# Optimization experiments

Hardware: AMD Instinct MI355X
Metric: run time of the kernel (lower is better)

## Reference

```python
import jax, jax.numpy as jnp
import numpy as np

N = 8192   # nodes
K = 64     # spectrum bins
DK = 64    # d_k == input_dim F'
G = 16     # num propagation modes
TAU = 1.0


def setup_inputs() -> dict:
    key = jax.random.key(0)
    ks = jax.random.split(key, 15)
    r = lambda k, sh, sc=1.0: jax.random.normal(k, sh, jnp.float32) * sc
    return {
        'z_n': r(ks[0], (N, DK)),
        'P_ref': r(ks[1], (N, K)),
        'P_in': r(ks[2], (N, K)),
        'A_ref': r(ks[3], (N, K)),
        'A_in': r(ks[4], (N, K)),
        'R_nm': r(ks[5], (N, N), 0.01),
        # learned params (torch nn.Linear stores weight as [out, in]; y = x @ W.T + b)
        'W_ind_w': r(ks[6], (DK, DK), 1.0 / np.sqrt(DK)),
        'W_ind_b': jnp.zeros((DK,), jnp.float32),
        'W_gate_w': r(ks[7], (DK, DK), 1.0 / np.sqrt(DK)),
        'W_gate_b': jnp.zeros((DK,), jnp.float32),
        'W_sys_w': r(ks[8], (DK, 2), 1.0 / np.sqrt(2.0)),
        'W_sys_b': jnp.zeros((DK,), jnp.float32),
        'W_s': r(ks[9], (G, DK, DK)),  # nn.Parameter(torch.randn(...))
        'W_k_w': r(ks[10], (DK, DK * DK), 1.0 / DK),
        'W_k_b': jnp.zeros((DK,), jnp.float32),
    }


def _delta(X_in, X_ref):
    # delta[i] = mean_{j,k} (X_in[j,k] - X_ref[i,k])^2 -> [N, 1]
    # (faithful to the broadcasted [N,N,K] mean in the torch code, computed
    #  via the expanded quadratic so the N^2*K tensor is never materialized)
    Kf = jnp.float32(X_in.shape[1])
    m_in2 = jnp.mean(X_in * X_in)              # scalar mean over j,k of X_in^2
    m_in = jnp.mean(X_in, axis=0)              # [K] mean over j
    d = m_in2 - 2.0 * (X_ref @ m_in) / Kf + jnp.mean(X_ref * X_ref, axis=1)
    return d[:, None]


def reference(z_n, P_ref, P_in, A_ref, A_in, R_nm,
              W_ind_w, W_ind_b, W_gate_w, W_gate_b,
              W_sys_w, W_sys_b, W_s, W_k_w, W_k_b):
    dP = _delta(P_in, P_ref)                                    # [N,1]
    dA = _delta(A_in, A_ref)                                    # [N,1]
    gate = jax.nn.sigmoid(z_n @ W_gate_w.T + W_gate_b)          # [N,DK]
    sys_feat = jnp.concatenate([dA, dP], axis=1) @ W_sys_w.T + W_sys_b
    q_n = z_n @ W_ind_w.T + W_ind_b + gate * sys_feat           # [N,DK]
    k_g = W_s.reshape(W_s.shape[0], -1) @ W_k_w.T + W_k_b       # [G,DK]
    s_ng = (q_n @ k_g.T) / jnp.sqrt(jnp.float32(DK))            # [N,G]
    u = jax.random.uniform(jax.random.key(42), s_ng.shape, jnp.float32)
    gumbel = -jnp.log(-jnp.log(u + 1e-10) + 1e-10)
    alpha = jax.nn.softmax((s_ng + gumbel) / TAU, axis=-1)      # [N,G]
    # fused: sum_g alpha[n,g] * (W_s[g] @ z_n[n])
    propagated = jnp.einsum('ng,gij,nj->ni', alpha, W_s, z_n)   # [N,DK]
    h_n = jax.nn.leaky_relu(R_nm @ propagated, negative_slope=0.01)
    return (h_n, s_ng)
```

## Files before the change

### kernel.cpp

```cpp
#include <hip/hip_runtime.h>
#include <hip/hip_bf16.h>
#include <stdint.h>

#define NN 8192

typedef __attribute__((ext_vector_type(8))) __bf16 bf16x8;
typedef __attribute__((ext_vector_type(4))) float f32x4;

#define WS_KG    192
#define WS_ALPHA 1216
#define WS_PT_BYTE 529408
#define WS_PART  394496
#define WS_KGP   427776

__device__ __forceinline__ void threefry2x32(uint32_t x0, uint32_t x1,
                                             uint32_t& o0, uint32_t& o1) {
  const uint32_t k0 = 0u, k1 = 42u;
  const uint32_t k2 = k0 ^ k1 ^ 0x1BD11BDAu;
  x0 += k0; x1 += k1;
#define TF_R(r) { x0 += x1; x1 = (x1 << (r)) | (x1 >> (32 - (r))); x1 ^= x0; }
  TF_R(13) TF_R(15) TF_R(26) TF_R(6)
  x0 += k1; x1 += k2 + 1u;
  TF_R(17) TF_R(29) TF_R(16) TF_R(24)
  x0 += k2; x1 += k0 + 2u;
  TF_R(13) TF_R(15) TF_R(26) TF_R(6)
  x0 += k0; x1 += k1 + 3u;
  TF_R(17) TF_R(29) TF_R(16) TF_R(24)
  x0 += k1; x1 += k2 + 4u;
  TF_R(13) TF_R(15) TF_R(26) TF_R(6)
  x0 += k2; x1 += k0 + 5u;
#undef TF_R
  o0 = x0; o1 = x1;
}

__device__ __forceinline__ bf16x8 cvt8(const float* __restrict__ p) {
  float4 a = *(const float4*)p;
  float4 b = *(const float4*)(p + 4);
  bf16x8 r;
  r[0] = (__bf16)a.x; r[1] = (__bf16)a.y; r[2] = (__bf16)a.z; r[3] = (__bf16)a.w;
  r[4] = (__bf16)b.x; r[5] = (__bf16)b.y; r[6] = (__bf16)b.z; r[7] = (__bf16)b.w;
  return r;
}

__device__ __forceinline__ bf16x8 cvt8g(const float* p) {
  float4 a = *(const float4*)p;
  float4 b = *(const float4*)(p + 4);
  bf16x8 r;
  r[0] = (__bf16)a.x; r[1] = (__bf16)a.y; r[2] = (__bf16)a.z; r[3] = (__bf16)a.w;
  r[4] = (__bf16)b.x; r[5] = (__bf16)b.y; r[6] = (__bf16)b.z; r[7] = (__bf16)b.w;
  return r;
}

__global__ __launch_bounds__(256) void k1_partial(const float* __restrict__ Pin,
                                                  const float* __restrict__ Ain,
                                                  float* __restrict__ ws) {
  __shared__ float scp[64], sca[64], ssq[2];
  int t = threadIdx.x, b = blockIdx.x;
  if (t < 64) { scp[t] = 0.f; sca[t] = 0.f; }
  if (t < 2) ssq[t] = 0.f;
  __syncthreads();
  const float4* P4 = (const float4*)Pin;
  const float4* A4 = (const float4*)Ain;
  float sp = 0.f, sa = 0.f;
  float cp0 = 0, cp1 = 0, cp2 = 0, cp3 = 0, ca0 = 0, ca1 = 0, ca2 = 0, ca3 = 0;
  int base = b * 512 + t;
#pragma unroll
  for (int k = 0; k < 2; ++k) {
    float4 p = P4[base + k * 256], a = A4[base + k * 256];
    sp += p.x * p.x + p.y * p.y + p.z * p.z + p.w * p.w;
    sa += a.x * a.x + a.y * a.y + a.z * a.z + a.w * a.w;
    cp0 += p.x; cp1 += p.y; cp2 += p.z; cp3 += p.w;
    ca0 += a.x; ca1 += a.y; ca2 += a.z; ca3 += a.w;
  }
  int c0 = (t * 4) & 63;
  atomicAdd(&scp[c0 + 0], cp0); atomicAdd(&scp[c0 + 1], cp1);
  atomicAdd(&scp[c0 + 2], cp2); atomicAdd(&scp[c0 + 3], cp3);
  atomicAdd(&sca[c0 + 0], ca0); atomicAdd(&sca[c0 + 1], ca1);
  atomicAdd(&sca[c0 + 2], ca2); atomicAdd(&sca[c0 + 3], ca3);
  for (int off = 32; off; off >>= 1) {
    sp += __shfl_down(sp, off);
    sa += __shfl_down(sa, off);
  }
  if ((t & 63) == 0) { atomicAdd(&ssq[0], sp); atomicAdd(&ssq[1], sa); }
  __syncthreads();
  float* dst = ws + WS_PART + b * 130;
  if (t < 64) { dst[2 + t] = scp[t]; dst[66 + t] = sca[t]; }
  if (t == 0) { dst[0] = ssq[0]; dst[1] = ssq[1]; }
}

__global__ __launch_bounds__(256) void k2a_kgpart(const float* __restrict__ Wsflat,
                                                  const float* __restrict__ Wkw,
                                                  float* __restrict__ ws) {
  __shared__ float wkT[64][65];
  __shared__ float wsT[64][17];
  int t = threadIdx.x, b = blockIdx.x;
  int c0 = b * 64;
  for (int idx = t; idx < 1024; idx += 256) {
    int o = idx >> 4, c4 = idx & 15;
    float4 v = *(const float4*)(Wkw + o * 4096 + c0 + c4 * 4);
    wkT[c4 * 4 + 0][o] = v.x; wkT[c4 * 4 + 1][o] = v.y;
    wkT[c4 * 4 + 2][o] = v.z; wkT[c4 * 4 + 3][o] = v.w;
  }
  {
    int g = t >> 4, c4 = t & 15;
    float4 v = *(const float4*)(Wsflat + g * 4096 + c0 + c4 * 4);
    wsT[c4 * 4 + 0][g] = v.x; wsT[c4 * 4 + 1][g] = v.y;
    wsT[c4 * 4 + 2][g] = v.z; wsT[c4 * 4 + 3][g] = v.w;
  }
  __syncthreads();
  int o = t & 63, g0 = (t >> 6) * 4;
  float a0 = 0.f, a1 = 0.f, a2 = 0.f, a3 = 0.f;
#pragma unroll 8
  for (int j = 0; j < 64; ++j) {
    float wk = wkT[j][o];
    a0 += wk * wsT[j][g0 + 0];
    a1 += wk * wsT[j][g0 + 1];
    a2 += wk * wsT[j][g0 + 2];
    a3 += wk * wsT[j][g0 + 3];
  }
  float* dst = ws + WS_KGP + b * 1024;
  dst[(g0 + 0) * 64 + o] = a0; dst[(g0 + 1) * 64 + o] = a1;
  dst[(g0 + 2) * 64 + o] = a2; dst[(g0 + 3) * 64 + o] = a3;
}

__global__ __launch_bounds__(256) void k2b_reduce(const float* __restrict__ Wkb,
                                                  float* __restrict__ ws) {
  int g = blockIdx.x, t = threadIdx.x;
  if (g == 16) {
    if (t < 130) {
      float s = 0.f;
#pragma unroll 8
      for (int b = 0; b < 256; ++b) s += ws[WS_PART + b * 130 + t];
      if (t == 0) ws[0] = s;
      else if (t == 1) ws[1] = s;
      else if (t < 66) ws[64 + (t - 2)] = s;
      else ws[128 + (t - 66)] = s;
    }
    return;
  }
  __shared__ float red[4][64];
  int o = t & 63, bq = t >> 6;
  float s = 0.f;
#pragma unroll
  for (int b = bq * 16; b < bq * 16 + 16; ++b)
    s += ws[WS_KGP + b * 1024 + g * 64 + o];
  red[bq][o] = s;
  __syncthreads();
  if (bq == 0)
    ws[WS_KG + g * 64 + o] = red[0][o] + red[1][o] + red[2][o] + red[3][o] + Wkb[o];
}

__global__ __launch_bounds__(256) void k3_fused(
    const float* __restrict__ z, const float* __restrict__ Pref,
    const float* __restrict__ Aref,
    const float* __restrict__ Wind_w, const float* __restrict__ Wind_b,
    const float* __restrict__ Wgate_w, const float* __restrict__ Wgate_b,
    const float* __restrict__ Wsys_w, const float* __restrict__ Wsys_b,
    float* __restrict__ ws, float* __restrict__ out_s) {
  int t = threadIdx.x, wv = t >> 6, lane = t & 63;
  int lg = lane >> 4, lm = lane & 15;
  int nb = blockIdx.x * 32 + wv * 8;
  __shared__ float qs[4][16][68];
  __shared__ float dpa[4][2][16];
  {
    int nl = lane >> 3, qt = lane & 7;
    const float4* pr4 = (const float4*)(Pref + (nb + nl) * 64 + qt * 8);
    const float4* ar4 = (const float4*)(Aref + (nb + nl) * 64 + qt * 8);
    const float4* mp4 = (const float4*)(ws + 64 + qt * 8);
    const float4* ma4 = (const float4*)(ws + 128 + qt * 8);
    float s1p = 0, s2p = 0, s1a = 0, s2a = 0;
#pragma unroll
    for (int j = 0; j < 2; ++j) {
      float4 p = pr4[j], a = ar4[j], mp = mp4[j], ma = ma4[j];
      s1p += p.x * mp.x + p.y * mp.y + p.z * mp.z + p.w * mp.w;
      s2p += p.x * p.x + p.y * p.y + p.z * p.z + p.w * p.w;
      s1a += a.x * ma.x + a.y * ma.y + a.z * ma.z + a.w * ma.w;
      s2a += a.x * a.x + a.y * a.y + a.z * a.z + a.w * a.w;
    }
    s1p += __shfl_xor(s1p, 1); s1p += __shfl_xor(s1p, 2); s1p += __shfl_xor(s1p, 4);
    s2p += __shfl_xor(s2p, 1); s2p += __shfl_xor(s2p, 2); s2p += __shfl_xor(s2p, 4);
    s1a += __shfl_xor(s1a, 1); s1a += __shfl_xor(s1a, 2); s1a += __shfl_xor(s1a, 4);
    s2a += __shfl_xor(s2a, 1); s2a += __shfl_xor(s2a, 2); s2a += __shfl_xor(s2a, 4);
    float m2P = ws[0] * (1.0f / 524288.0f);
    float m2A = ws[1] * (1.0f / 524288.0f);
    float dP = m2P - s1p * (2.0f / (64.0f * 8192.0f)) + s2p * (1.0f / 64.0f);
    float dA = m2A - s1a * (2.0f / (64.0f * 8192.0f)) + s2a * (1.0f / 64.0f);
    if (qt == 0) { dpa[wv][0][nl] = dP; dpa[wv][1][nl] = dA; }
    if (qt == 1) { dpa[wv][0][8 + nl] = 0.f; dpa[wv][1][8 + nl] = 0.f; }
  }
  int zrow = nb + lm; if (zrow > 8191) zrow = 8191;
  bf16x8 az[2];
#pragma unroll
  for (int h = 0; h < 2; ++h)
    az[h] = cvt8(z + zrow * 64 + h * 32 + lg * 8);
  f32x4 accg[4], acci[4];
#pragma unroll
  for (int ii = 0; ii < 4; ++ii) {
    f32x4 cg = {0.f, 0.f, 0.f, 0.f}, ci = {0.f, 0.f, 0.f, 0.f};
#pragma unroll
    for (int h = 0; h < 2; ++h) {
      bf16x8 bg = cvt8(Wgate_w + (ii * 16 + lm) * 64 + h * 32 + lg * 8);
      bf16x8 bi = cvt8(Wind_w + (ii * 16 + lm) * 64 + h * 32 + lg * 8);
      cg = __builtin_amdgcn_mfma_f32_16x16x32_bf16(az[h], bg, cg, 0, 0, 0);
      ci = __builtin_amdgcn_mfma_f32_16x16x32_bf16(az[h], bi, ci, 0, 0, 0);
    }
    accg[ii] = cg; acci[ii] = ci;
  }
  __syncthreads();
#pragma unroll
  for (int ii = 0; ii < 4; ++ii) {
    int o = ii * 16 + lm;
    float bg = Wgate_b[o], bi = Wind_b[o], bs = Wsys_b[o];
    float w0 = Wsys_w[o * 2], w1 = Wsys_w[o * 2 + 1];
#pragma unroll
    for (int r = 0; r < 4; ++r) {
      int node = lg * 4 + r;
      float dP = dpa[wv][0][node], dA = dpa[wv][1][node];
      float gate = 1.0f / (1.0f + expf(-(accg[ii][r] + bg)));
      float sys = dA * w0 + dP * w1 + bs;
      qs[wv][node][o] = acci[ii][r] + bi + gate * sys;
    }
  }
  __syncthreads();
  bf16x8 aq[2], bq[2];
#pragma unroll
  for (int h = 0; h < 2; ++h) {
    aq[h] = cvt8g(&qs[wv][lm][h * 32 + lg * 8]);
    bq[h] = cvt8g(ws + WS_KG + lm * 64 + h * 32 + lg * 8);
  }
  f32x4 accs = {0.f, 0.f, 0.f, 0.f};
  accs = __builtin_amdgcn_mfma_f32_16x16x32_bf16(aq[0], bq[0], accs, 0, 0, 0);
  accs = __builtin_amdgcn_mfma_f32_16x16x32_bf16(aq[1], bq[1], accs, 0, 0, 0);
  if (lg < 2) {
#pragma unroll
    for (int r = 0; r < 4; ++r) {
      int n = nb + lg * 4 + r;
      float sv = accs[r] * 0.125f;
      uint32_t idx = (uint32_t)(n * 16 + lm);
      uint32_t r0_, r1_;
      threefry2x32(0u, idx, r0_, r1_);
      uint32_t bits = r0_ ^ r1_;
      float u = __uint_as_float((bits >> 9) | 0x3f800000u) - 1.0f;
      float gum = -logf(-logf(u + 1e-10f) + 1e-10f);
      float tv = sv + gum;
      float mx = tv;
      mx = fmaxf(mx, __shfl_xor(mx, 1)); mx = fmaxf(mx, __shfl_xor(mx, 2));
      mx = fmaxf(mx, __shfl_xor(mx, 4)); mx = fmaxf(mx, __shfl_xor(mx, 8));
      float e = expf(tv - mx);
      float se = e;
      se += __shfl_xor(se, 1); se += __shfl_xor(se, 2);
      se += __shfl_xor(se, 4); se += __shfl_xor(se, 8);
      out_s[n * 16 + lm] = sv;
      ws[WS_ALPHA + n * 16 + lm] = e / se;
    }
  }
}

__global__ __launch_bounds__(256) void k4_prop(const float* __restrict__ z,
                                               const float* __restrict__ Ws,
                                               const float* __restrict__ alpha_ws,
                                               __bf16* __restrict__ PT) {
  int t = threadIdx.x, wv = t >> 6, lane = t & 63;
  int lg = lane >> 4, lm = lane & 15;
  int n0 = blockIdx.x * 32;
  __shared__ float al[32][16];
  al[t >> 4][t & 15] = alpha_ws[n0 * 16 + t];
  al[16 + (t >> 4)][t & 15] = alpha_ws[n0 * 16 + 256 + t];
  __syncthreads();
  bf16x8 af[2][2];
#pragma unroll
  for (int m = 0; m < 2; ++m)
#pragma unroll
    for (int h = 0; h < 2; ++h)
      af[m][h] = cvt8(z + (n0 + m * 16 + lm) * 64 + h * 32 + lg * 8);
  int i0 = wv * 16;
  f32x4 prop[2] = {{0.f, 0.f, 0.f, 0.f}, {0.f, 0.f, 0.f, 0.f}};
  for (int g = 0; g < 16; ++g) {
    bf16x8 bf[2];
#pragma unroll
    for (int h = 0; h < 2; ++h)
      bf[h] = cvt8(Ws + g * 4096 + (i0 + lm) * 64 + h * 32 + lg * 8);
#pragma unroll
    for (int m = 0; m < 2; ++m) {
      f32x4 tf = {0.f, 0.f, 0.f, 0.f};
      tf = __builtin_amdgcn_mfma_f32_16x16x32_bf16(af[m][0], bf[0], tf, 0, 0, 0);
      tf = __builtin_amdgcn_mfma_f32_16x16x32_bf16(af[m][1], bf[1], tf, 0, 0, 0);
#pragma unroll
      for (int r = 0; r < 4; ++r)
        prop[m][r] += al[m * 16 + lg * 4 + r][g] * tf[r];
    }
  }
#pragma unroll
  for (int m = 0; m < 2; ++m)
#pragma unroll
    for (int r = 0; r < 4; ++r)
      PT[(i0 + lm) * 8192 + n0 + m * 16 + lg * 4 + r] = (__bf16)prop[m][r];
}

__global__ __launch_bounds__(512) void k5_gemm(const float* __restrict__ R,
                                               const __bf16* __restrict__ PT,
                                               float* __restrict__ out) {
  __shared__ float lds[2][16][516];
  int t = threadIdx.x, wv = t >> 6, lane = t & 63;
  int lg = lane >> 4, lm = lane & 15;
  int row0 = blockIdx.x * 16;
  int srow[4], scol[4];
#pragma unroll
  for (int r = 0; r < 4; ++r) {
    int idx = r * 512 + t;
    srow[r] = idx >> 7;
    scol[r] = (idx & 127) * 4;
  }
  const float* Rb = R + (size_t)row0 * 8192;
  f32x4 acc[4];
#pragma unroll
  for (int ii = 0; ii < 4; ++ii) acc[ii] = {0.f, 0.f, 0.f, 0.f};
  float4 stg[4];
#pragma unroll
  for (int r = 0; r < 4; ++r)
    stg[r] = *(const float4*)(Rb + (size_t)srow[r] * 8192 + scol[r]);
#pragma unroll
  for (int r = 0; r < 4; ++r)
    *(float4*)&lds[0][srow[r]][scol[r]] = stg[r];
  __syncthreads();
  for (int tile = 0; tile < 16; ++tile) {
    int cur = tile & 1;
    if (tile < 15) {
#pragma unroll
      for (int r = 0; r < 4; ++r)
        stg[r] = *(const float4*)(Rb + (size_t)srow[r] * 8192 + (tile + 1) * 512 + scol[r]);
    }
#pragma unroll
    for (int ks = 0; ks < 2; ++ks) {
      int kc = wv * 64 + ks * 32 + lg * 8;
      bf16x8 a = cvt8g(&lds[cur][lm][kc]);
      int kglob = tile * 512 + kc;
#pragma unroll
      for (int ii = 0; ii < 4; ++ii) {
        bf16x8 b = *(const bf16x8*)(PT + (ii * 16 + lm) * 8192 + kglob);
        acc[ii] = __builtin_amdgcn_mfma_f32_16x16x32_bf16(a, b, acc[ii], 0, 0, 0);
      }
    }
    if (tile < 15) {
#pragma unroll
      for (int r = 0; r < 4; ++r)
        *(float4*)&lds[cur ^ 1][srow[r]][scol[r]] = stg[r];
    }
    __syncthreads();
  }
  float* red = &lds[0][0][0];
#pragma unroll
  for (int ii = 0; ii < 4; ++ii)
#pragma unroll
    for (int r = 0; r < 4; ++r)
      red[wv * 1024 + (lg * 4 + r) * 64 + ii * 16 + lm] = acc[ii][r];
  __syncthreads();
  for (int e = t; e < 1024; e += 512) {
    int rr = e >> 6, cc = e & 63;
    float v = 0.f;
#pragma unroll
    for (int w = 0; w < 8; ++w) v += red[w * 1024 + rr * 64 + cc];
    v = v > 0.f ? v : 0.01f * v;
    out[(row0 + rr) * 64 + cc] = v;
  }
}

extern "C" void kernel_launch(void* const* d_in, const int* in_sizes, int n_in,
                              void* d_out, int out_size, void* d_ws, size_t ws_size,
                              hipStream_t stream) {
  const float* z      = (const float*)d_in[0];
  const float* Pref   = (const float*)d_in[1];
  const float* Pin    = (const float*)d_in[2];
  const float* Aref   = (const float*)d_in[3];
  const float* Ain    = (const float*)d_in[4];
  const float* R      = (const float*)d_in[5];
  const float* Wind_w = (const float*)d_in[6];
  const float* Wind_b = (const float*)d_in[7];
  const float* Wgate_w= (const float*)d_in[8];
  const float* Wgate_b= (const float*)d_in[9];
  const float* Wsys_w = (const float*)d_in[10];
  const float* Wsys_b = (const float*)d_in[11];
  const float* Ws     = (const float*)d_in[12];
  const float* Wkw    = (const float*)d_in[13];
  const float* Wkb    = (const float*)d_in[14];
  float* out = (float*)d_out;
  float* ws  = (float*)d_ws;
  __bf16* PT = (__bf16*)((char*)d_ws + WS_PT_BYTE);

  k1_partial<<<256, 256, 0, stream>>>(Pin, Ain, ws);
  k2a_kgpart<<<64, 256, 0, stream>>>(Ws, Wkw, ws);
  k2b_reduce<<<17, 256, 0, stream>>>(Wkb, ws);
  k3_fused<<<256, 256, 0, stream>>>(z, Pref, Aref, Wind_w, Wind_b, Wgate_w,
                                    Wgate_b, Wsys_w, Wsys_b, ws, out + 524288);
  k4_prop<<<256, 256, 0, stream>>>(z, Ws, ws + WS_ALPHA, PT);
  k5_gemm<<<512, 512, 0, stream>>>(R, PT, out);
}
```

Baseline: 128.1 us.

## Fuse gating/softmax kernel with propagation kernel; stage R tile as bf16 in LDS

Merges the score/gumbel-softmax kernel with the mode-propagation kernel, so alpha stays in shared memory instead of making a round trip through the global workspace, and one launch is removed. Separately, the R-GEMM kernel now converts R to bf16 when writing its shared-memory tile rather than when reading it back. This halves LDS footprint and read traffic for the A operand. The fused kernel carries more registers and LDS, which may reduce occupancy.

```diff
diff --git a/kernel.cpp b/kernel.cpp
--- a/kernel.cpp
+++ b/kernel.cpp
@@ -5,10 +5,10 @@
 #define NN 8192
 
 typedef __attribute__((ext_vector_type(8))) __bf16 bf16x8;
+typedef __attribute__((ext_vector_type(4))) __bf16 bf16x4;
 typedef __attribute__((ext_vector_type(4))) float f32x4;
 
 #define WS_KG    192
-#define WS_ALPHA 1216
 #define WS_PT_BYTE 529408
 #define WS_PART  394496
 #define WS_KGP   427776
@@ -51,6 +51,12 @@
   return r;
 }
 
+__device__ __forceinline__ void st4bf(__bf16* p, float4 v) {
+  bf16x4 b;
+  b[0] = (__bf16)v.x; b[1] = (__bf16)v.y; b[2] = (__bf16)v.z; b[3] = (__bf16)v.w;
+  *(bf16x4*)p = b;
+}
+
 __global__ __launch_bounds__(256) void k1_partial(const float* __restrict__ Pin,
                                                   const float* __restrict__ Ain,
                                                   float* __restrict__ ws) {
@@ -150,18 +156,22 @@
     ws[WS_KG + g * 64 + o] = red[0][o] + red[1][o] + red[2][o] + red[3][o] + Wkb[o];
 }
 
-__global__ __launch_bounds__(256) void k3_fused(
+__global__ __launch_bounds__(256) void k34_fused(
     const float* __restrict__ z, const float* __restrict__ Pref,
     const float* __restrict__ Aref,
     const float* __restrict__ Wind_w, const float* __restrict__ Wind_b,
     const float* __restrict__ Wgate_w, const float* __restrict__ Wgate_b,
     const float* __restrict__ Wsys_w, const float* __restrict__ Wsys_b,
-    float* __restrict__ ws, float* __restrict__ out_s) {
+    const float* __restrict__ Ws,
+    const float* __restrict__ ws, float* __restrict__ out_s,
+    __bf16* __restrict__ PT) {
   int t = threadIdx.x, wv = t >> 6, lane = t & 63;
   int lg = lane >> 4, lm = lane & 15;
-  int nb = blockIdx.x * 32 + wv * 8;
+  int n0 = blockIdx.x * 32;
+  int nb = n0 + wv * 8;
   __shared__ float qs[4][16][68];
   __shared__ float dpa[4][2][16];
+  __shared__ float al_lds[32][16];
   {
     int nl = lane >> 3, qt = lane & 7;
     const float4* pr4 = (const float4*)(Pref + (nb + nl) * 64 + qt * 8);
@@ -222,50 +232,40 @@
     }
   }
   __syncthreads();
-  bf16x8 aq[2], bq[2];
-#pragma unroll
-  for (int h = 0; h < 2; ++h) {
-    aq[h] = cvt8g(&qs[wv][lm][h * 32 + lg * 8]);
-    bq[h] = cvt8g(ws + WS_KG + lm * 64 + h * 32 + lg * 8);
-  }
-  f32x4 accs = {0.f, 0.f, 0.f, 0.f};
-  accs = __builtin_amdgcn_mfma_f32_16x16x32_bf16(aq[0], bq[0], accs, 0, 0, 0);
-  accs = __builtin_amdgcn_mfma_f32_16x16x32_bf16(aq[1], bq[1], accs, 0, 0, 0);
-  if (lg < 2) {
-#pragma unroll
-    for (int r = 0; r < 4; ++r) {
-      int n = nb + lg * 4 + r;
-      float sv = accs[r] * 0.125f;
-      uint32_t idx = (uint32_t)(n * 16 + lm);
-      uint32_t r0_, r1_;
-      threefry2x32(0u, idx, r0_, r1_);
-      uint32_t bits = r0_ ^ r1_;
-      float u = __uint_as_float((bits >> 9) | 0x3f800000u) - 1.0f;
-      float gum = -logf(-logf(u + 1e-10f) + 1e-10f);
-      float tv = sv + gum;
-      float mx = tv;
-      mx = fmaxf(mx, __shfl_xor(mx, 1)); mx = fmaxf(mx, __shfl_xor(mx, 2));
-      mx = fmaxf(mx, __shfl_xor(mx, 4)); mx = fmaxf(mx, __shfl_xor(mx, 8));
-      float e = expf(tv - mx);
-      float se = e;
-      se += __shfl_xor(se, 1); se += __shfl_xor(se, 2);
-      se += __shfl_xor(se, 4); se += __shfl_xor(se, 8);
-      out_s[n * 16 + lm] = sv;
-      ws[WS_ALPHA + n * 16 + lm] = e / se;
-    }
-  }
-}
-
-__global__ __launch_bounds__(256) void k4_prop(const float* __restrict__ z,
-                                               const float* __restrict__ Ws,
-                                               const float* __restrict__ alpha_ws,
-                                               __bf16* __restrict__ PT) {
-  int t = threadIdx.x, wv = t >> 6, lane = t & 63;
-  int lg = lane >> 4, lm = lane & 15;
-  int n0 = blockIdx.x * 32;
-  __shared__ float al[32][16];
-  al[t >> 4][t & 15] = alpha_ws[n0 * 16 + t];
-  al[16 + (t >> 4)][t & 15] = alpha_ws[n0 * 16 + 256 + t];
+  {
+    bf16x8 aq[2], bq[2];
+#pragma unroll
+    for (int h = 0; h < 2; ++h) {
+      aq[h] = cvt8g(&qs[wv][lm][h * 32 + lg * 8]);
+      bq[h] = cvt8g(ws + WS_KG + lm * 64 + h * 32 + lg * 8);
+    }
+    f32x4 accs = {0.f, 0.f, 0.f, 0.f};
+    accs = __builtin_amdgcn_mfma_f32_16x16x32_bf16(aq[0], bq[0], accs, 0, 0, 0);
+    accs = __builtin_amdgcn_mfma_f32_16x16x32_bf16(aq[1], bq[1], accs, 0, 0, 0);
+    if (lg < 2) {
+#pragma unroll
+      for (int r = 0; r < 4; ++r) {
+        int n = nb + lg * 4 + r;
+        float sv = accs[r] * 0.125f;
+        uint32_t idx = (uint32_t)(n * 16 + lm);
+        uint32_t r0_, r1_;
+        threefry2x32(0u, idx, r0_, r1_);
+        uint32_t bits = r0_ ^ r1_;
+        float u = __uint_as_float((bits >> 9) | 0x3f800000u) - 1.0f;
+        float gum = -logf(-logf(u + 1e-10f) + 1e-10f);
+        float tv = sv + gum;
+        float mx = tv;
+        mx = fmaxf(mx, __shfl_xor(mx, 1)); mx = fmaxf(mx, __shfl_xor(mx, 2));
+        mx = fmaxf(mx, __shfl_xor(mx, 4)); mx = fmaxf(mx, __shfl_xor(mx, 8));
+        float e = expf(tv - mx);
+        float se = e;
+        se += __shfl_xor(se, 1); se += __shfl_xor(se, 2);
+        se += __shfl_xor(se, 4); se += __shfl_xor(se, 8);
+        out_s[n * 16 + lm] = sv;
+        al_lds[wv * 8 + lg * 4 + r][lm] = e / se;
+      }
+    }
+  }
   __syncthreads();
   bf16x8 af[2][2];
 #pragma unroll
@@ -287,7 +287,7 @@
       tf = __builtin_amdgcn_mfma_f32_16x16x32_bf16(af[m][1], bf[1], tf, 0, 0, 0);
 #pragma unroll
       for (int r = 0; r < 4; ++r)
-        prop[m][r] += al[m * 16 + lg * 4 + r][g] * tf[r];
+        prop[m][r] += al_lds[m * 16 + lg * 4 + r][g] * tf[r];
     }
   }
 #pragma unroll
@@ -300,7 +300,7 @@
 __global__ __launch_bounds__(512) void k5_gemm(const float* __restrict__ R,
                                                const __bf16* __restrict__ PT,
                                                float* __restrict__ out) {
-  __shared__ float lds[2][16][516];
+  __shared__ __bf16 lds[2][16][520];
   int t = threadIdx.x, wv = t >> 6, lane = t & 63;
   int lg = lane >> 4, lm = lane & 15;
   int row0 = blockIdx.x * 16;
@@ -321,7 +321,7 @@
     stg[r] = *(const float4*)(Rb + (size_t)srow[r] * 8192 + scol[r]);
 #pragma unroll
   for (int r = 0; r < 4; ++r)
-    *(float4*)&lds[0][srow[r]][scol[r]] = stg[r];
+    st4bf(&lds[0][srow[r]][scol[r]], stg[r]);
   __syncthreads();
   for (int tile = 0; tile < 16; ++tile) {
     int cur = tile & 1;
@@ -333,7 +333,7 @@
 #pragma unroll
     for (int ks = 0; ks < 2; ++ks) {
       int kc = wv * 64 + ks * 32 + lg * 8;
-      bf16x8 a = cvt8g(&lds[cur][lm][kc]);
+      bf16x8 a = *(const bf16x8*)&lds[cur][lm][kc];
       int kglob = tile * 512 + kc;
 #pragma unroll
       for (int ii = 0; ii < 4; ++ii) {
@@ -344,11 +344,11 @@
     if (tile < 15) {
 #pragma unroll
       for (int r = 0; r < 4; ++r)
-        *(float4*)&lds[cur ^ 1][srow[r]][scol[r]] = stg[r];
+        st4bf(&lds[cur ^ 1][srow[r]][scol[r]], stg[r]);
     }
     __syncthreads();
   }
-  float* red = &lds[0][0][0];
+  float* red = (float*)&lds[0][0][0];
 #pragma unroll
   for (int ii = 0; ii < 4; ++ii)
 #pragma unroll
@@ -390,8 +390,8 @@
   k1_partial<<<256, 256, 0, stream>>>(Pin, Ain, ws);
   k2a_kgpart<<<64, 256, 0, stream>>>(Ws, Wkw, ws);
   k2b_reduce<<<17, 256, 0, stream>>>(Wkb, ws);
-  k3_fused<<<256, 256, 0, stream>>>(z, Pref, Aref, Wind_w, Wind_b, Wgate_w,
-                                    Wgate_b, Wsys_w, Wsys_b, ws, out + 524288);
-  k4_prop<<<256, 256, 0, stream>>>(z, Ws, ws + WS_ALPHA, PT);
+  k34_fused<<<256, 256, 0, stream>>>(z, Pref, Aref, Wind_w, Wind_b, Wgate_w,
+                                     Wgate_b, Wsys_w, Wsys_b, Ws, ws,
+                                     out + 524288, PT);
   k5_gemm<<<512, 512, 0, stream>>>(R, PT, out);
 }
```

Measured after the change: 129.5 us. No clear change (+1.1%).
